# Kernel tuning notes

Measured on AMD Instinct MI355X. Metric: run time of the kernel, lower is better.

Reference implementation:

```python
import jax, jax.numpy as jnp
import numpy as np

H = 1024
NH = 16
HD = H // NH  # 64


def setup_inputs() -> dict:
    key = jax.random.key(0)
    ks = jax.random.split(key, 8)
    B, S = 4, 1024
    scale = 1.0 / np.sqrt(H)
    return {
        "hidden_states": jax.random.normal(ks[0], (B, S, H), jnp.float32),
        "attention_mask": jnp.ones((B, S), jnp.float32),
        "Wq": jax.random.normal(ks[1], (H, H), jnp.float32) * scale,
        "bq": jnp.zeros((H,), jnp.float32),
        "Wk": jax.random.normal(ks[2], (H, H), jnp.float32) * scale,
        "bk": jnp.zeros((H,), jnp.float32),
        "Wv": jax.random.normal(ks[3], (H, H), jnp.float32) * scale,
        "bv": jnp.zeros((H,), jnp.float32),
        "Wo": jax.random.normal(ks[4], (H, H), jnp.float32) * scale,
        "bo": jnp.zeros((H,), jnp.float32),
    }


def _split_heads(x):
    # [B,S,H] -> [B,NH,S,HD]
    B, S, _ = x.shape
    return x.reshape(B, S, NH, HD).transpose(0, 2, 1, 3)


def reference(hidden_states, attention_mask, Wq, bq, Wk, bk, Wv, bv, Wo, bo):
    B, S, _ = hidden_states.shape
    q = _split_heads(hidden_states @ Wq.T + bq)  # [B,NH,S,HD]
    k = _split_heads(hidden_states @ Wk.T + bk)
    v = _split_heads(hidden_states @ Wv.T + bv)
    scores = jnp.einsum("bhqd,bhkd->bhqk", q, k) / jnp.sqrt(jnp.float32(HD))
    # additive mask: (1 - mask) * -10000, broadcast [B,1,1,S]
    scores = scores + (1.0 - attention_mask)[:, None, None, :] * -10000.0
    probs = jax.nn.softmax(scores, axis=-1)  # dropout is identity at eval
    ctx = jnp.einsum("bhqk,bhkd->bhqd", probs, v)
    ctx = ctx.transpose(0, 2, 1, 3).reshape(B, S, H)
    out = ctx @ Wo.T + bo
    return (out, probs)
```

## Files before the change

### kernel.cpp

```cpp
#include <hip/hip_runtime.h>
#include <hip/hip_bf16.h>


typedef __attribute__((ext_vector_type(8))) short short8;
typedef __attribute__((ext_vector_type(4))) float f32x4;
typedef __attribute__((ext_vector_type(4))) short short4v;

#define LOG2E 1.44269504f
#define MFMA_BF16(a, b, c) __builtin_amdgcn_mfma_f32_16x16x32_bf16((a), (b), (c), 0, 0, 0)

__device__ __forceinline__ short f2bf(float x) {
    __hip_bfloat16 h = __float2bfloat16(x);
    return __builtin_bit_cast(short, h);
}
__device__ __forceinline__ float bf2f(short s) {
    __hip_bfloat16 h = __builtin_bit_cast(__hip_bfloat16, s);
    return __bfloat162float(h);
}

__device__ __forceinline__ void gload16(const void* g, void* lds) {
    __builtin_amdgcn_global_load_lds(
        (const __attribute__((address_space(1))) void*)g,
        (__attribute__((address_space(3))) void*)lds, 16, 0, 0);
}

__global__ __launch_bounds__(256) void cvt_bf16_kernel(const float* __restrict__ src,
                                                       short* __restrict__ dst, int n8) {
    int i = blockIdx.x * 256 + threadIdx.x;
    if (i >= n8) return;
    const float4* s = (const float4*)src;
    float4 a = s[i * 2], b = s[i * 2 + 1];
    short8 o;
    o[0] = f2bf(a.x); o[1] = f2bf(a.y); o[2] = f2bf(a.z); o[3] = f2bf(a.w);
    o[4] = f2bf(b.x); o[5] = f2bf(b.y); o[6] = f2bf(b.z); o[7] = f2bf(b.w);
    *(short8*)(dst + (size_t)i * 8) = o;
}

__global__ __launch_bounds__(256) void cvt4_kernel(const float* __restrict__ s0,
                                                   const float* __restrict__ s1,
                                                   const float* __restrict__ s2,
                                                   const float* __restrict__ s3,
                                                   short* __restrict__ dst) {
    int sel = blockIdx.x >> 9;
    const float* srcs[4] = {s0, s1, s2, s3};
    const float* s = srcs[sel];
    int li = (blockIdx.x & 511) * 256 + threadIdx.x;
    const float4* sp = (const float4*)s;
    float4 a = sp[li * 2], b = sp[li * 2 + 1];
    short8 o;
    o[0] = f2bf(a.x); o[1] = f2bf(a.y); o[2] = f2bf(a.z); o[3] = f2bf(a.w);
    o[4] = f2bf(b.x); o[5] = f2bf(b.y); o[6] = f2bf(b.z); o[7] = f2bf(b.w);
    *(short8*)(dst + ((size_t)sel * 131072 + li) * 8) = o;
}

template <int EPI>
__global__ __launch_bounds__(256) void gemm128_kernel(
    const short* __restrict__ A, const short* __restrict__ B,
    float* __restrict__ Cf, const float* __restrict__ bias0,
    short* __restrict__ qhi, short* __restrict__ qlo,
    short* __restrict__ khi, short* __restrict__ klo, short* __restrict__ vt,
    const float* __restrict__ biasq, const float* __restrict__ biask,
    const float* __restrict__ biasv)
{
    __shared__ short smem[16384];
    int tid = threadIdx.x;
    int l = tid & 63, w = tid >> 6;
    int lr = l & 15, lg = l >> 4;
    int wm = w >> 1, wn = w & 1;
    int m0 = blockIdx.y * 128, n0 = blockIdx.x * 128;

    f32x4 acc[4][4] = {};

    int sr = l >> 2;
    int sc = (l & 3) * 16;
    const char* Ag = (const char*)A + ((size_t)(m0 + w * 32 + sr) * 1024) * 2 + sc;
    const char* Bg = (const char*)B + ((size_t)(n0 + w * 32 + sr) * 1024) * 2 + sc;

    auto stage = [&](int buf, int t) {
        int kb = t * 64;
        #pragma unroll
        for (int g = 0; g < 2; ++g) {
            gload16(Ag + (size_t)g * (16 * 2048) + kb,
                    (char*)&smem[buf * 4096 + (w * 32 + g * 16) * 32]);
            gload16(Bg + (size_t)g * (16 * 2048) + kb,
                    (char*)&smem[8192 + buf * 4096 + (w * 32 + g * 16) * 32]);
        }
    };

    stage(0, 0);
    __syncthreads();

    int cur = 0;
    for (int t = 0; t < 32; ++t) {
        if (t < 31) stage(cur ^ 1, t + 1);
        short8 a[4], b[4];
        #pragma unroll
        for (int i = 0; i < 4; ++i)
            a[i] = *(const short8*)&smem[cur * 4096 + (wm * 64 + i * 16 + lr) * 32 + lg * 8];
        #pragma unroll
        for (int j = 0; j < 4; ++j)
            b[j] = *(const short8*)&smem[8192 + cur * 4096 + (wn * 64 + j * 16 + lr) * 32 + lg * 8];
        #pragma unroll
        for (int i = 0; i < 4; ++i)
            #pragma unroll
            for (int j = 0; j < 4; ++j)
                acc[i][j] = MFMA_BF16(a[i], b[j], acc[i][j]);
        __syncthreads();
        cur ^= 1;
    }

    if (EPI == 0) {
        #pragma unroll
        for (int i = 0; i < 4; ++i) {
            int m_base = m0 + wm * 64 + i * 16 + lg * 4;
            #pragma unroll
            for (int j = 0; j < 4; ++j) {
                int n = n0 + wn * 64 + j * 16 + lr;
                float bv = bias0[n];
                #pragma unroll
                for (int r = 0; r < 4; ++r)
                    Cf[(size_t)(m_base + r) * 1024 + n] = acc[i][j][r] + bv;
            }
        }
    } else {
        int sel = n0 >> 10;
        int nb = n0 & 1023;
        if (sel == 2) {
            #pragma unroll
            for (int i = 0; i < 4; ++i) {
                int ml = wm * 64 + i * 16 + lg * 4;
                #pragma unroll
                for (int j = 0; j < 4; ++j) {
                    int nl = wn * 64 + j * 16 + lr;
                    float bvv = biasv[nb + nl];
                    short4v o;
                    #pragma unroll
                    for (int r = 0; r < 4; ++r) o[r] = f2bf(acc[i][j][r] + bvv);
                    *(short4v*)((char*)smem + nl * 256 + ((ml * 2) ^ ((nl & 7) << 4))) = o;
                }
            }
            __syncthreads();
            int b_ = m0 >> 10, s0 = m0 & 1023;
            #pragma unroll
            for (int it = 0; it < 8; ++it) {
                int idx = it * 256 + tid;
                int nrow = idx >> 4, c8 = idx & 15;
                short8 vv = *(const short8*)((char*)smem + nrow * 256 +
                                             ((c8 * 16) ^ ((nrow & 7) << 4)));
                int ng = nb + nrow;
                int h = ng >> 6, d = ng & 63;
                *(short8*)(vt + (size_t)((b_ * 16 + h) * 64 + d) * 1024 + s0 + c8 * 8) = vv;
            }
        } else {
            short* Chi = sel ? khi : qhi;
            short* Clo = sel ? klo : qlo;
            const float* bias = sel ? biask : biasq;
            float ps = sel ? 1.0f : 0.125f;
            #pragma unroll
            for (int hv = 0; hv < 2; ++hv) {
                __syncthreads();
                #pragma unroll
                for (int i = 0; i < 4; ++i) {
                    int ml = wm * 64 + i * 16 + lg * 4;
                    #pragma unroll
                    for (int j = 0; j < 4; ++j) {
                        int nl = wn * 64 + j * 16 + lr;
                        float bvv = bias[nb + nl];
                        #pragma unroll
                        for (int r = 0; r < 4; ++r) {
                            float v = (acc[i][j][r] + bvv) * ps;
                            short hh = f2bf(v);
                            short ss = hv ? f2bf(v - bf2f(hh)) : hh;
                            smem[(ml + r) * 128 + nl] = ss;
                        }
                    }
                }
                __syncthreads();
                short* dst = hv ? Clo : Chi;
                #pragma unroll
                for (int it = 0; it < 8; ++it) {
                    int idx = it * 256 + tid;
                    int row = idx >> 4, c8 = idx & 15;
                    short8 vv = *(const short8*)&smem[row * 128 + c8 * 8];
                    *(short8*)(dst + (size_t)(m0 + row) * 1024 + nb + c8 * 8) = vv;
                }
            }
        }
    }
}

__global__ __launch_bounds__(256) void attn_fused_kernel(
    const short* __restrict__ Qhi, const short* __restrict__ Qlo,
    const short* __restrict__ Khi, const short* __restrict__ Klo,
    const float* __restrict__ mask, float* __restrict__ P,
    const short* __restrict__ vt, short* __restrict__ ctxb)
{
    constexpr int P_O = 0, KHI_O = 0, KLO_O = 16384, QHI_O = 32768, QLO_O = 36864,
                  MADD_O = 65536, WRM_O = 69632, WRL_O = 70144;
    __shared__ __align__(16) char lds[70656];

    int tid = threadIdx.x;
    int l = tid & 63, w = tid >> 6;
    int c = l & 15, g = l >> 4;
    int z = blockIdx.y;
    int b = z >> 4, h = z & 15;
    int qb = blockIdx.x;

    {
        const float4* mrow = (const float4*)(mask + b * 1024);
        float4 mm = mrow[tid];
        float4 md;
        md.x = (1.0f - mm.x) * -10000.0f;
        md.y = (1.0f - mm.y) * -10000.0f;
        md.z = (1.0f - mm.z) * -10000.0f;
        md.w = (1.0f - mm.w) * -10000.0f;
        *(float4*)(lds + MADD_O + tid * 16) = md;
    }

    {
        int r_ = w * 8 + (l >> 3);
        int ul = (l & 7) ^ (r_ & 7);
        size_t gq = ((size_t)(b * 1024 + qb * 32 + r_)) * 1024 + h * 64 + ul * 8;
        gload16(Qhi + gq, lds + QHI_O + w * 1024);
        gload16(Qlo + gq, lds + QLO_O + w * 1024);
    }
    asm volatile("s_waitcnt vmcnt(0)" ::: "memory");
    __syncthreads();

    short8 bqh[2][2], bql[2][2];
    #pragma unroll
    for (int qt = 0; qt < 2; ++qt) {
        int row = qt * 16 + c;
        #pragma unroll
        for (int dt = 0; dt < 2; ++dt) {
            int u = (dt * 4 + g) ^ (row & 7);
            bqh[qt][dt] = *(const short8*)(lds + QHI_O + row * 128 + u * 16);
            bql[qt][dt] = *(const short8*)(lds + QLO_O + row * 128 + u * 16);
        }
    }

    f32x4 acc[8][2][2] = {};

    #pragma unroll
    for (int cc = 0; cc < 8; ++cc) {
        #pragma unroll
        for (int i = 0; i < 4; ++i) {
            int r_ = i * 32 + w * 8 + (l >> 3);
            int ul = (l & 7) ^ (r_ & 7);
            size_t gk = ((size_t)(b * 1024 + cc * 128 + r_)) * 1024 + h * 64 + ul * 8;
            gload16(Khi + gk, lds + KHI_O + i * 4096 + w * 1024);
            gload16(Klo + gk, lds + KLO_O + i * 4096 + w * 1024);
        }
        asm volatile("s_waitcnt vmcnt(0)" ::: "memory");
        __syncthreads();

        #pragma unroll
        for (int kt = 0; kt < 2; ++kt) {
            int row = w * 32 + kt * 16 + c;
            #pragma unroll
            for (int dt = 0; dt < 2; ++dt) {
                int u = (dt * 4 + g) ^ (row & 7);
                short8 ah = *(const short8*)(lds + KHI_O + row * 128 + u * 16);
                short8 al = *(const short8*)(lds + KLO_O + row * 128 + u * 16);
                #pragma unroll
                for (int qt = 0; qt < 2; ++qt) {
                    acc[cc][kt][qt] = MFMA_BF16(ah, bqh[qt][dt], acc[cc][kt][qt]);
                    acc[cc][kt][qt] = MFMA_BF16(ah, bql[qt][dt], acc[cc][kt][qt]);
                    acc[cc][kt][qt] = MFMA_BF16(al, bqh[qt][dt], acc[cc][kt][qt]);
                }
            }
        }
        __syncthreads();
    }

    float mx[2] = {-3.0e38f, -3.0e38f};
    #pragma unroll
    for (int cc = 0; cc < 8; ++cc)
        #pragma unroll
        for (int kt = 0; kt < 2; ++kt) {
            f32x4 md = *(const f32x4*)(lds + MADD_O + (cc * 128 + w * 32 + kt * 16 + g * 4) * 4);
            #pragma unroll
            for (int qt = 0; qt < 2; ++qt) {
                f32x4 v = acc[cc][kt][qt] + md;
                acc[cc][kt][qt] = v;
                mx[qt] = fmaxf(mx[qt], fmaxf(fmaxf(v[0], v[1]), fmaxf(v[2], v[3])));
            }
        }
    #pragma unroll
    for (int qt = 0; qt < 2; ++qt) {
        mx[qt] = fmaxf(mx[qt], __shfl_xor(mx[qt], 16));
        mx[qt] = fmaxf(mx[qt], __shfl_xor(mx[qt], 32));
    }
    float* wrm = (float*)(lds + WRM_O);
    float* wrl = (float*)(lds + WRL_O);
    if (g == 0) { wrm[w * 32 + c] = mx[0]; wrm[w * 32 + 16 + c] = mx[1]; }
    __syncthreads();
    float mfin[2];
    mfin[0] = fmaxf(fmaxf(wrm[c], wrm[32 + c]), fmaxf(wrm[64 + c], wrm[96 + c]));
    mfin[1] = fmaxf(fmaxf(wrm[16 + c], wrm[48 + c]), fmaxf(wrm[80 + c], wrm[112 + c]));

    float sum[2] = {0.0f, 0.0f};
    #pragma unroll
    for (int cc = 0; cc < 8; ++cc)
        #pragma unroll
        for (int kt = 0; kt < 2; ++kt)
            #pragma unroll
            for (int qt = 0; qt < 2; ++qt) {
                f32x4 v = acc[cc][kt][qt];
                v[0] = exp2f((v[0] - mfin[qt]) * LOG2E);
                v[1] = exp2f((v[1] - mfin[qt]) * LOG2E);
                v[2] = exp2f((v[2] - mfin[qt]) * LOG2E);
                v[3] = exp2f((v[3] - mfin[qt]) * LOG2E);
                acc[cc][kt][qt] = v;
                sum[qt] += (v[0] + v[1]) + (v[2] + v[3]);
            }
    #pragma unroll
    for (int qt = 0; qt < 2; ++qt) {
        sum[qt] += __shfl_xor(sum[qt], 16);
        sum[qt] += __shfl_xor(sum[qt], 32);
    }
    if (g == 0) { wrl[w * 32 + c] = sum[0]; wrl[w * 32 + 16 + c] = sum[1]; }
    __syncthreads();
    float inv[2];
    inv[0] = 1.0f / ((wrl[c] + wrl[32 + c]) + (wrl[64 + c] + wrl[96 + c]));
    inv[1] = 1.0f / ((wrl[16 + c] + wrl[48 + c]) + (wrl[80 + c] + wrl[112 + c]));

    float* Pz = P + ((size_t)z << 20);
    #pragma unroll
    for (int cc = 0; cc < 8; ++cc)
        #pragma unroll
        for (int kt = 0; kt < 2; ++kt)
            #pragma unroll
            for (int qt = 0; qt < 2; ++qt) {
                f32x4 v = acc[cc][kt][qt];
                v[0] *= inv[qt]; v[1] *= inv[qt]; v[2] *= inv[qt]; v[3] *= inv[qt];
                int q = qt * 16 + c;
                int k = cc * 128 + w * 32 + kt * 16 + g * 4;
                *(f32x4*)(Pz + (size_t)(qb * 32 + q) * 1024 + k) = v;
                short4v ps4;
                ps4[0] = f2bf(v[0]); ps4[1] = f2bf(v[1]);
                ps4[2] = f2bf(v[2]); ps4[3] = f2bf(v[3]);
                *(short4v*)(lds + P_O + q * 2048 + ((k * 2) ^ ((q & 7) << 4))) = ps4;
            }
    __syncthreads();

    {
        const short* vbase = vt + (size_t)z * 65536 + (size_t)(w * 16 + c) * 1024 + g * 8;
        f32x4 pacc[2] = {};
        short8 vfrag = *(const short8*)vbase;
        for (int kc = 0; kc < 32; ++kc) {
            short8 vnext = {};
            if (kc < 31) vnext = *(const short8*)(vbase + (kc + 1) * 32);
            short8 pa[2];
            #pragma unroll
            for (int qt = 0; qt < 2; ++qt) {
                int q = qt * 16 + c;
                int kbyte = kc * 64 + g * 16;
                pa[qt] = *(const short8*)(lds + P_O + q * 2048 + (kbyte ^ ((q & 7) << 4)));
            }
            pacc[0] = MFMA_BF16(pa[0], vfrag, pacc[0]);
            pacc[1] = MFMA_BF16(pa[1], vfrag, pacc[1]);
            vfrag = vnext;
        }
        #pragma unroll
        for (int qt = 0; qt < 2; ++qt) {
            int s = qb * 32 + qt * 16 + g * 4;
            size_t base = ((size_t)b * 1024 + s) * 1024 + h * 64 + w * 16 + c;
            #pragma unroll
            for (int r = 0; r < 4; ++r)
                ctxb[base + (size_t)r * 1024] = f2bf(pacc[qt][r]);
        }
    }
}

extern "C" void kernel_launch(void* const* d_in, const int* in_sizes, int n_in,
                              void* d_out, int out_size, void* d_ws, size_t ws_size,
                              hipStream_t stream) {
    const float* hs   = (const float*)d_in[0];
    const float* mask = (const float*)d_in[1];
    const float* Wq   = (const float*)d_in[2];
    const float* bq   = (const float*)d_in[3];
    const float* Wk   = (const float*)d_in[4];
    const float* bk   = (const float*)d_in[5];
    const float* Wv   = (const float*)d_in[6];
    const float* bv   = (const float*)d_in[7];
    const float* Wo   = (const float*)d_in[8];
    const float* bo   = (const float*)d_in[9];

    float* out   = (float*)d_out;
    float* probs = out + 4194304;

    char* ws = (char*)d_ws;
    short* qhi  = (short*)(ws);
    short* qlo  = (short*)(ws + (8u << 20));
    short* khi  = (short*)(ws + (16u << 20));
    short* klo  = (short*)(ws + (24u << 20));
    short* vt   = (short*)(ws + (32u << 20));
    short* ctxb = (short*)(ws + (40u << 20));
    short* hsb  = (short*)(ws + (48u << 20));
    short* wcat = (short*)(ws + (56u << 20));
    short* wob  = wcat + 3 * (1u << 20);

    dim3 blk(256);

    cvt_bf16_kernel<<<2048, blk, 0, stream>>>(hs, hsb, 524288);
    cvt4_kernel<<<2048, blk, 0, stream>>>(Wq, Wk, Wv, Wo, wcat);

    gemm128_kernel<1><<<dim3(24, 32), blk, 0, stream>>>(
        hsb, wcat, nullptr, nullptr, qhi, qlo, khi, klo, vt, bq, bk, bv);

    attn_fused_kernel<<<dim3(32, 64), blk, 0, stream>>>(qhi, qlo, khi, klo, mask, probs,
                                                        vt, ctxb);

    gemm128_kernel<0><<<dim3(8, 32), blk, 0, stream>>>(
        ctxb, wob, out, bo, nullptr, nullptr, nullptr, nullptr, nullptr,
        nullptr, nullptr, nullptr);
}
```

Measured before the change: 211.1 us.

## Double-buffer K staging per warp and load Q and mask directly from global

K tiles are now double-buffered in LDS. Each warp stages only the rows it consumes, so the per-chunk __syncthreads can be replaced by vmcnt waits that overlap the next chunk's loads with the current MFMAs. Q fragments and the additive mask are read straight from global memory into registers instead of going through LDS, which removes the initial barrier and frees LDS. The trade-off is more global loads for the mask and uncoalesced Q reads.

```diff
diff --git a/kernel.cpp b/kernel.cpp
--- a/kernel.cpp
+++ b/kernel.cpp
@@ -195,9 +195,8 @@
     const float* __restrict__ mask, float* __restrict__ P,
     const short* __restrict__ vt, short* __restrict__ ctxb)
 {
-    constexpr int P_O = 0, KHI_O = 0, KLO_O = 16384, QHI_O = 32768, QLO_O = 36864,
-                  MADD_O = 65536, WRM_O = 69632, WRL_O = 70144;
-    __shared__ __align__(16) char lds[70656];
+    constexpr int P_O = 0, WRM_O = 65536, WRL_O = 66048;
+    __shared__ __align__(16) char lds[66560];
 
     int tid = threadIdx.x;
     int l = tid & 63, w = tid >> 6;
@@ -206,62 +205,52 @@
     int b = z >> 4, h = z & 15;
     int qb = blockIdx.x;
 
-    {
-        const float4* mrow = (const float4*)(mask + b * 1024);
-        float4 mm = mrow[tid];
-        float4 md;
-        md.x = (1.0f - mm.x) * -10000.0f;
-        md.y = (1.0f - mm.y) * -10000.0f;
-        md.z = (1.0f - mm.z) * -10000.0f;
-        md.w = (1.0f - mm.w) * -10000.0f;
-        *(float4*)(lds + MADD_O + tid * 16) = md;
-    }
-
-    {
-        int r_ = w * 8 + (l >> 3);
-        int ul = (l & 7) ^ (r_ & 7);
-        size_t gq = ((size_t)(b * 1024 + qb * 32 + r_)) * 1024 + h * 64 + ul * 8;
-        gload16(Qhi + gq, lds + QHI_O + w * 1024);
-        gload16(Qlo + gq, lds + QLO_O + w * 1024);
-    }
-    asm volatile("s_waitcnt vmcnt(0)" ::: "memory");
-    __syncthreads();
-
     short8 bqh[2][2], bql[2][2];
     #pragma unroll
     for (int qt = 0; qt < 2; ++qt) {
         int row = qt * 16 + c;
         #pragma unroll
         for (int dt = 0; dt < 2; ++dt) {
-            int u = (dt * 4 + g) ^ (row & 7);
-            bqh[qt][dt] = *(const short8*)(lds + QHI_O + row * 128 + u * 16);
-            bql[qt][dt] = *(const short8*)(lds + QLO_O + row * 128 + u * 16);
-        }
-    }
-
-    f32x4 acc[8][2][2] = {};
-
-    #pragma unroll
-    for (int cc = 0; cc < 8; ++cc) {
+            size_t gq = ((size_t)(b * 1024 + qb * 32 + row)) * 1024 + h * 64 + (dt * 4 + g) * 8;
+            bqh[qt][dt] = *(const short8*)(Qhi + gq);
+            bql[qt][dt] = *(const short8*)(Qlo + gq);
+        }
+    }
+    asm volatile("s_waitcnt vmcnt(0)" ::: "memory");
+
+    auto stageK = [&](int buf, int cc) {
+        int r0 = w * 32;
         #pragma unroll
         for (int i = 0; i < 4; ++i) {
-            int r_ = i * 32 + w * 8 + (l >> 3);
+            int r_ = r0 + i * 8 + (l >> 3);
             int ul = (l & 7) ^ (r_ & 7);
             size_t gk = ((size_t)(b * 1024 + cc * 128 + r_)) * 1024 + h * 64 + ul * 8;
-            gload16(Khi + gk, lds + KHI_O + i * 4096 + w * 1024);
-            gload16(Klo + gk, lds + KLO_O + i * 4096 + w * 1024);
-        }
-        asm volatile("s_waitcnt vmcnt(0)" ::: "memory");
-        __syncthreads();
-
+            gload16(Khi + gk, lds + buf * 32768 + (r0 + i * 8) * 128);
+            gload16(Klo + gk, lds + buf * 32768 + 16384 + (r0 + i * 8) * 128);
+        }
+    };
+
+    f32x4 acc[8][2][2] = {};
+
+    stageK(0, 0);
+    #pragma unroll
+    for (int cc = 0; cc < 8; ++cc) {
+        if (cc < 7) {
+            stageK((cc + 1) & 1, cc + 1);
+            asm volatile("s_waitcnt vmcnt(8)" ::: "memory");
+        } else {
+            asm volatile("s_waitcnt vmcnt(0)" ::: "memory");
+        }
+        __builtin_amdgcn_sched_barrier(0);
+        const char* kb = lds + (cc & 1) * 32768;
         #pragma unroll
         for (int kt = 0; kt < 2; ++kt) {
             int row = w * 32 + kt * 16 + c;
             #pragma unroll
             for (int dt = 0; dt < 2; ++dt) {
                 int u = (dt * 4 + g) ^ (row & 7);
-                short8 ah = *(const short8*)(lds + KHI_O + row * 128 + u * 16);
-                short8 al = *(const short8*)(lds + KLO_O + row * 128 + u * 16);
+                short8 ah = *(const short8*)(kb + row * 128 + u * 16);
+                short8 al = *(const short8*)(kb + 16384 + row * 128 + u * 16);
                 #pragma unroll
                 for (int qt = 0; qt < 2; ++qt) {
                     acc[cc][kt][qt] = MFMA_BF16(ah, bqh[qt][dt], acc[cc][kt][qt]);
@@ -270,15 +259,21 @@
                 }
             }
         }
-        __syncthreads();
-    }
-
+    }
+
+    const float* mrow = mask + b * 1024;
     float mx[2] = {-3.0e38f, -3.0e38f};
     #pragma unroll
     for (int cc = 0; cc < 8; ++cc)
         #pragma unroll
         for (int kt = 0; kt < 2; ++kt) {
-            f32x4 md = *(const f32x4*)(lds + MADD_O + (cc * 128 + w * 32 + kt * 16 + g * 4) * 4);
+            int k = cc * 128 + w * 32 + kt * 16 + g * 4;
+            float4 mm = *(const float4*)(mrow + k);
+            f32x4 md;
+            md[0] = (1.0f - mm.x) * -10000.0f;
+            md[1] = (1.0f - mm.y) * -10000.0f;
+            md[2] = (1.0f - mm.z) * -10000.0f;
+            md[3] = (1.0f - mm.w) * -10000.0f;
             #pragma unroll
             for (int qt = 0; qt < 2; ++qt) {
                 f32x4 v = acc[cc][kt][qt] + md;
```

New measurement: 246.8 us. +16.9%, slower.
